# Kernel optimization log

Measured on AMD Instinct MI355X. Metric: run time of the kernel, lower is better.

The kernel has to match this reference:

```python
import jax, jax.numpy as jnp
import numpy as np

N = 100_000      # nodes
E = 1_600_000    # edges (avg degree 16)
C_IN = 32
C_OUT = 32


def setup_inputs() -> dict:
    key = jax.random.key(0)
    ks = jax.random.split(key, 8)
    x = jax.random.normal(ks[0], (N, C_IN), jnp.float32)
    edge_index = jax.random.randint(ks[1], (2, E), 0, N)
    edge_weight = jax.random.uniform(ks[2], (E,), jnp.float32)
    h = jax.random.normal(ks[3], (N, C_OUT), jnp.float32)
    s_in = 1.0 / np.sqrt(C_IN)
    s_out = 1.0 / np.sqrt(C_OUT)
    # 6 ChebConvs (gates z, r, h-tilde; each has an x-conv and an h-conv), K=2
    Wx = jax.random.normal(ks[4], (3, 2, C_IN, C_OUT), jnp.float32) * s_in
    bx = jnp.zeros((3, C_OUT), jnp.float32)
    Wh = jax.random.normal(ks[5], (3, 2, C_OUT, C_OUT), jnp.float32) * s_out
    bh = jnp.zeros((3, C_OUT), jnp.float32)
    Wl = jax.random.normal(ks[6], (C_OUT, 1), jnp.float32) * s_out
    bl = jnp.zeros((1,), jnp.float32)
    return dict(x=x, edge_index=edge_index, edge_weight=edge_weight, h=h,
                Wx=Wx, bx=bx, Wh=Wh, bh=bh, Wl=Wl, bl=bl)


def _cheb(v, W, b, coef, src, dst, n):
    # ChebConv, K=2, sym norm, lambda_max=2:
    #   T0 = v ; T1 = Lhat @ v, Lhat = -D^{-1/2} A D^{-1/2} (zero diagonal)
    t1 = jax.ops.segment_sum(coef[:, None] * v[src], dst, num_segments=n)
    return v @ W[0] + t1 @ W[1] + b


def reference(x, edge_index, edge_weight, h, Wx, bx, Wh, bh, Wl, bl):
    n = x.shape[0]
    src, dst = edge_index[0], edge_index[1]
    deg = jax.ops.segment_sum(edge_weight, src, num_segments=n)
    safe = jnp.where(deg > 0, deg, 1.0)
    dis = jnp.where(deg > 0, jax.lax.rsqrt(safe), 0.0)
    coef = -(dis[src] * edge_weight * dis[dst])  # scaled-Laplacian edge coeffs

    def gate(g, v_x, v_h):
        return (_cheb(v_x, Wx[g], bx[g], coef, src, dst, n)
                + _cheb(v_h, Wh[g], bh[g], coef, src, dst, n))

    z = jax.nn.sigmoid(gate(0, x, h))          # update gate
    r = jax.nn.sigmoid(gate(1, x, h))          # reset gate
    h_tilde = jnp.tanh(gate(2, x, h * r))      # candidate state
    h_new = z * h + (1.0 - z) * h_tilde
    out = jax.nn.softplus(jax.nn.relu(h_new) @ Wl + bl)  # [N, 1]
    return (out, h_new)
```

## Files before the change

kernel.cpp:

```cpp
#include <hip/hip_runtime.h>
#include <math.h>

#define NN 100000
#define NE 1600000
#define C  32
#define CAP 48

#define BSH    8
#define BNODES 256
#define NB     392
#define BCAP   4608
#define EPB    4096

#define WQ_SCALE 32767.0f
#define INV_WQ   (1.0f/32767.0f)
#define DEG_FIX  4194304.0f
#define INV_DEG_FIX (1.0f/4194304.0f)

typedef __attribute__((ext_vector_type(8))) short short8;
typedef __attribute__((ext_vector_type(4))) float floatx4;

__device__ __forceinline__ unsigned rn_bf16(float f) {
    unsigned b = __float_as_uint(f);
    return (b + 0x7fffu + ((b >> 16) & 1u)) >> 16;
}

__device__ __forceinline__ float sigm(float a) { return 1.f / (1.f + expf(-a)); }

__device__ __forceinline__ unsigned enc_edge(int s, float w) {
    int wq = (int)(w * WQ_SCALE + 0.5f);
    wq = wq > 32767 ? 32767 : wq;
    return ((unsigned)s << 15) | (unsigned)wq;
}

__device__ __forceinline__ short8 pack_hi8(uint4 a, uint4 b) {
    short8 v;
    v[0] = (short)(a.x >> 16); v[1] = (short)(a.y >> 16);
    v[2] = (short)(a.z >> 16); v[3] = (short)(a.w >> 16);
    v[4] = (short)(b.x >> 16); v[5] = (short)(b.y >> 16);
    v[6] = (short)(b.z >> 16); v[7] = (short)(b.w >> 16);
    return v;
}
__device__ __forceinline__ short8 pack_lo8(uint4 a, uint4 b) {
    short8 v;
    v[0] = (short)(a.x & 0xffffu); v[1] = (short)(a.y & 0xffffu);
    v[2] = (short)(a.z & 0xffffu); v[3] = (short)(a.w & 0xffffu);
    v[4] = (short)(b.x & 0xffffu); v[5] = (short)(b.y & 0xffffu);
    v[6] = (short)(b.z & 0xffffu); v[7] = (short)(b.w & 0xffffu);
    return v;
}

__global__ __launch_bounds__(256) void bin_pass(const int* __restrict__ ei,
                                                const float* __restrict__ w,
                                                int* __restrict__ gbin_d,
                                                int* __restrict__ gbin_s,
                                                uint2* __restrict__ drec,
                                                unsigned* __restrict__ srec) {
    __shared__ int hd[NB], hs[NB];
    __shared__ int sd[NB], ss[NB];
    __shared__ int bd[NB], bs[NB];
    __shared__ int cd[NB], cs[NB];
    __shared__ __align__(16) uint2 ld[EPB];
    __shared__ unsigned lsr[EPB];
    int tid = threadIdx.x;
    for (int i = tid; i < NB; i += 256) { hd[i] = 0; hs[i] = 0; }
    __syncthreads();
    int e0 = blockIdx.x * EPB;
    int m = min(EPB, NE - e0);
    for (int i = tid; i < m; i += 256) {
        atomicAdd(&hs[ei[e0 + i] >> BSH], 1);
        atomicAdd(&hd[ei[NE + e0 + i] >> BSH], 1);
    }
    __syncthreads();
    for (int i = tid; i < NB; i += 256) {
        bd[i] = hd[i] ? atomicAdd(&gbin_d[i], hd[i]) : 0;
        bs[i] = hs[i] ? atomicAdd(&gbin_s[i], hs[i]) : 0;
    }
    if (tid < 128) {
        const int* hh = (tid < 64) ? hd : hs;
        int* so = (tid < 64) ? sd : ss;
        int lane = tid & 63;
        int c0 = lane * 7;
        int vals[7]; int sum = 0;
#pragma unroll
        for (int q = 0; q < 7; ++q) {
            int idx = c0 + q;
            int v = (idx < NB) ? hh[idx] : 0;
            vals[q] = sum; sum += v;
        }
        int incl = sum;
#pragma unroll
        for (int off = 1; off < 64; off <<= 1) {
            int t = __shfl_up(incl, off, 64);
            if (lane >= off) incl += t;
        }
        int base = incl - sum;
#pragma unroll
        for (int q = 0; q < 7; ++q) {
            int idx = c0 + q;
            if (idx < NB) so[idx] = base + vals[q];
        }
    }
    __syncthreads();
    for (int i = tid; i < NB; i += 256) { cd[i] = sd[i]; cs[i] = ss[i]; }
    __syncthreads();
    for (int i = tid; i < m; i += 256) {
        int s = ei[e0 + i], d = ei[NE + e0 + i];
        float we = w[e0 + i];
        int p = atomicAdd(&cd[d >> BSH], 1);
        ld[p] = make_uint2(((unsigned)s << BSH) | (unsigned)(d & (BNODES - 1)),
                           __float_as_uint(we));
        int ps = atomicAdd(&cs[s >> BSH], 1);
        lsr[ps] = ((unsigned)(s & (BNODES - 1)) << 22) | (unsigned)(we * DEG_FIX);
    }
    __syncthreads();
    for (int i = tid; i < m; i += 256) {
        int lo = 0, hi = NB - 1;
        while (lo < hi) { int mid = (lo + hi + 1) >> 1; if (sd[mid] <= i) lo = mid; else hi = mid - 1; }
        int off = bd[lo] + (i - sd[lo]);
        if (off < BCAP) drec[(size_t)lo * BCAP + off] = ld[i];
        lo = 0; hi = NB - 1;
        while (lo < hi) { int mid = (lo + hi + 1) >> 1; if (ss[mid] <= i) lo = mid; else hi = mid - 1; }
        off = bs[lo] + (i - ss[lo]);
        if (off < BCAP) srec[(size_t)lo * BCAP + off] = lsr[i];
    }
}

__global__ __launch_bounds__(256) void bin_build(const uint2* __restrict__ drec,
                                                 const unsigned* __restrict__ srec,
                                                 const int* __restrict__ gbin_d,
                                                 const int* __restrict__ gbin_s,
                                                 const float* __restrict__ x,
                                                 const float* __restrict__ h,
                                                 unsigned* __restrict__ buckets,
                                                 int* __restrict__ cursor,
                                                 float* __restrict__ dis,
                                                 unsigned* __restrict__ xh2,
                                                 unsigned* __restrict__ xraw2) {
    __shared__ __align__(16) unsigned lbuck[BNODES * CAP];
    __shared__ int lcur[BNODES];
    __shared__ int ldeg[BNODES];
    __shared__ float sdis[BNODES];
    int b = blockIdx.x, tid = threadIdx.x;
    lcur[tid] = 0; ldeg[tid] = 0;
    __syncthreads();
    int cnt_d = min(gbin_d[b], BCAP);
    int cnt_s = min(gbin_s[b], BCAP);
    for (int i = tid; i < cnt_d; i += 256) {
        uint2 r = drec[(size_t)b * BCAP + i];
        int d8 = r.x & (BNODES - 1);
        int s  = (int)(r.x >> BSH);
        int pos = atomicAdd(&lcur[d8], 1);
        if (pos < CAP) lbuck[d8 * CAP + pos] = enc_edge(s, __uint_as_float(r.y));
    }
    for (int i = tid; i < cnt_s; i += 256) {
        unsigned r = srec[(size_t)b * BCAP + i];
        atomicAdd(&ldeg[r >> 22], (int)(r & 0x3FFFFFu));
    }
    __syncthreads();
    uint4* gb = (uint4*)(buckets + (size_t)b * BNODES * CAP);
    const uint4* lb = (const uint4*)lbuck;
    for (int i = tid; i < BNODES * CAP / 4; i += 256) gb[i] = lb[i];
    int n = b * BNODES + tid;
    float dv = 0.f;
    if (n < NN) {
        cursor[n] = lcur[tid];
        int di = ldeg[tid];
        dv = di > 0 ? rsqrtf((float)di * INV_DEG_FIX) : 0.f;
        dis[n] = dv;
    }
    sdis[tid] = dv;
    __syncthreads();
    size_t base = (size_t)b * BNODES * C;
    for (int i = tid; i < BNODES * C; i += 256) {
        size_t t = base + i;
        if (t < (size_t)NN * C) {
            float d = sdis[i >> 5];
            float xv = x[t], hv = h[t];
            xh2[t]   = (rn_bf16(xv * d) << 16) | rn_bf16(hv * d);
            xraw2[t] = (rn_bf16(xv) << 16) | rn_bf16(hv);
        }
    }
}

__global__ __launch_bounds__(256) void agg_xh(const unsigned* __restrict__ buckets,
                                              const int* __restrict__ cursor,
                                              const float* __restrict__ dis,
                                              const unsigned* __restrict__ xh2,
                                              unsigned* __restrict__ agg2) {
    int tid = threadIdx.x;
    int nl = tid >> 5, j = tid & 31;
    int n = blockIdx.x * 8 + nl;
    if (n >= NN) return;
    int cnt = min(cursor[n], CAP);
    float ax0 = 0.f, ax1 = 0.f, ax2 = 0.f, ax3 = 0.f;
    float ah0 = 0.f, ah1 = 0.f, ah2 = 0.f, ah3 = 0.f;
    for (int base = 0; base < cnt; base += 32) {
        int idx = base + j;
        int sv = 0; float cv = 0.f;
        if (idx < cnt) {
            unsigned u = buckets[(size_t)n * CAP + idx];
            sv = (int)(u >> 15);
            cv = (float)(u & 32767u) * INV_WQ;
        }
        int mm = min(32, cnt - base);
        int i2 = 0;
        for (; i2 + 8 <= mm; i2 += 8) {
            float vx[8], vh[8], cc[8];
#pragma unroll
            for (int q = 0; q < 8; ++q) {
                int s = __shfl(sv, i2 + q, 32);
                cc[q] = __shfl(cv, i2 + q, 32);
                unsigned u = xh2[(size_t)s * C + j];
                vx[q] = __uint_as_float(u & 0xffff0000u);
                vh[q] = __uint_as_float(u << 16);
            }
            ax0 = fmaf(cc[0], vx[0], ax0); ah0 = fmaf(cc[0], vh[0], ah0);
            ax1 = fmaf(cc[1], vx[1], ax1); ah1 = fmaf(cc[1], vh[1], ah1);
            ax2 = fmaf(cc[2], vx[2], ax2); ah2 = fmaf(cc[2], vh[2], ah2);
            ax3 = fmaf(cc[3], vx[3], ax3); ah3 = fmaf(cc[3], vh[3], ah3);
            ax0 = fmaf(cc[4], vx[4], ax0); ah0 = fmaf(cc[4], vh[4], ah0);
            ax1 = fmaf(cc[5], vx[5], ax1); ah1 = fmaf(cc[5], vh[5], ah1);
            ax2 = fmaf(cc[6], vx[6], ax2); ah2 = fmaf(cc[6], vh[6], ah2);
            ax3 = fmaf(cc[7], vx[7], ax3); ah3 = fmaf(cc[7], vh[7], ah3);
        }
        for (; i2 < mm; ++i2) {
            int s = __shfl(sv, i2, 32); float cf = __shfl(cv, i2, 32);
            unsigned u = xh2[(size_t)s * C + j];
            ax0 = fmaf(cf, __uint_as_float(u & 0xffff0000u), ax0);
            ah0 = fmaf(cf, __uint_as_float(u << 16), ah0);
        }
    }
    float disn = -dis[n];
    float ax = disn * ((ax0 + ax1) + (ax2 + ax3));
    float ah = disn * ((ah0 + ah1) + (ah2 + ah3));
    agg2[(size_t)n * C + j] = (rn_bf16(ax) << 16) | rn_bf16(ah);
}

__global__ __launch_bounds__(256) void gate_mfma(const unsigned* __restrict__ xraw2,
                                                 const unsigned* __restrict__ agg2,
                                                 const float* __restrict__ dis,
                                                 const float* __restrict__ Wx,
                                                 const float* __restrict__ Wh,
                                                 const float* __restrict__ bx,
                                                 const float* __restrict__ bh,
                                                 unsigned* __restrict__ hrz2,
                                                 unsigned short* __restrict__ hr16,
                                                 float* __restrict__ pout) {
    __shared__ __align__(16) unsigned short Bl[20][64][8];
    int tid = threadIdx.x;
    for (int i = tid; i < 20 * 64; i += 256) {
        int f = i >> 6, l = i & 63;
        int t, c;
        if (f < 16) { t = f >> 2; c = f & 3; }
        else        { t = 4 + ((f - 16) >> 1); c = (f - 16) & 1; }
        int g = t >> 1;
        int j = ((t & 1) << 4) + (l & 15);
        int kb = (l >> 4) << 3;
        const float* srcp = (c < 2 ? Wx : Wh) + g * 2048 + (c & 1) * 1024 + j;
        unsigned pk[4];
#pragma unroll
        for (int q = 0; q < 4; ++q) {
            unsigned lo = rn_bf16(srcp[(kb + 2 * q) * 32]);
            unsigned hi = rn_bf16(srcp[(kb + 2 * q + 1) * 32]);
            pk[q] = (hi << 16) | lo;
        }
        *(uint4*)(&Bl[f][l][0]) = make_uint4(pk[0], pk[1], pk[2], pk[3]);
    }

    int lane = tid & 63, wave = tid >> 6;
    int j0 = lane & 15, quad = lane >> 4;
    int tbase = blockIdx.x * 64 + wave * 16;
    int na = tbase + j0;
    short8 A0 = {0,0,0,0,0,0,0,0}, A1 = A0, A2 = A0, A3 = A0;
    if (na < NN) {
        const uint4* px = (const uint4*)(xraw2 + (size_t)na * C + quad * 8);
        uint4 xa = px[0], xb = px[1];
        A0 = pack_hi8(xa, xb);
        A2 = pack_lo8(xa, xb);
        const uint4* pg = (const uint4*)(agg2 + (size_t)na * C + quad * 8);
        uint4 ga = pg[0], gb = pg[1];
        A1 = pack_hi8(ga, gb);
        A3 = pack_lo8(ga, gb);
    }
    __syncthreads();

#define B8(f) (*(const short8*)(&Bl[f][lane][0]))
    floatx4 az0 = {0.f,0.f,0.f,0.f}, az1 = az0, ar0 = az0, ar1 = az0, ap0 = az0, ap1 = az0;
    az0 = __builtin_amdgcn_mfma_f32_16x16x32_bf16(A0, B8(0),  az0, 0, 0, 0);
    az0 = __builtin_amdgcn_mfma_f32_16x16x32_bf16(A1, B8(1),  az0, 0, 0, 0);
    az0 = __builtin_amdgcn_mfma_f32_16x16x32_bf16(A2, B8(2),  az0, 0, 0, 0);
    az0 = __builtin_amdgcn_mfma_f32_16x16x32_bf16(A3, B8(3),  az0, 0, 0, 0);
    az1 = __builtin_amdgcn_mfma_f32_16x16x32_bf16(A0, B8(4),  az1, 0, 0, 0);
    az1 = __builtin_amdgcn_mfma_f32_16x16x32_bf16(A1, B8(5),  az1, 0, 0, 0);
    az1 = __builtin_amdgcn_mfma_f32_16x16x32_bf16(A2, B8(6),  az1, 0, 0, 0);
    az1 = __builtin_amdgcn_mfma_f32_16x16x32_bf16(A3, B8(7),  az1, 0, 0, 0);
    ar0 = __builtin_amdgcn_mfma_f32_16x16x32_bf16(A0, B8(8),  ar0, 0, 0, 0);
    ar0 = __builtin_amdgcn_mfma_f32_16x16x32_bf16(A1, B8(9),  ar0, 0, 0, 0);
    ar0 = __builtin_amdgcn_mfma_f32_16x16x32_bf16(A2, B8(10), ar0, 0, 0, 0);
    ar0 = __builtin_amdgcn_mfma_f32_16x16x32_bf16(A3, B8(11), ar0, 0, 0, 0);
    ar1 = __builtin_amdgcn_mfma_f32_16x16x32_bf16(A0, B8(12), ar1, 0, 0, 0);
    ar1 = __builtin_amdgcn_mfma_f32_16x16x32_bf16(A1, B8(13), ar1, 0, 0, 0);
    ar1 = __builtin_amdgcn_mfma_f32_16x16x32_bf16(A2, B8(14), ar1, 0, 0, 0);
    ar1 = __builtin_amdgcn_mfma_f32_16x16x32_bf16(A3, B8(15), ar1, 0, 0, 0);
    ap0 = __builtin_amdgcn_mfma_f32_16x16x32_bf16(A0, B8(16), ap0, 0, 0, 0);
    ap0 = __builtin_amdgcn_mfma_f32_16x16x32_bf16(A1, B8(17), ap0, 0, 0, 0);
    ap1 = __builtin_amdgcn_mfma_f32_16x16x32_bf16(A0, B8(18), ap1, 0, 0, 0);
    ap1 = __builtin_amdgcn_mfma_f32_16x16x32_bf16(A1, B8(19), ap1, 0, 0, 0);
#undef B8

    float bza = bx[j0]      + bh[j0];
    float bzb = bx[j0 + 16] + bh[j0 + 16];
    float bra = bx[32 + j0] + bh[32 + j0];
    float brb = bx[48 + j0] + bh[48 + j0];
    float bpa = bx[64 + j0] + bh[64 + j0];
    float bpb = bx[80 + j0] + bh[80 + j0];
#pragma unroll
    for (int p = 0; p < 4; ++p) {
        int nr = tbase + quad * 4 + p;
        if (nr >= NN) continue;
        float dn = dis[nr];
        size_t ra = (size_t)nr * C + j0;
        size_t rb = ra + 16;
        float ha = __uint_as_float(xraw2[ra] << 16);
        float hb = __uint_as_float(xraw2[rb] << 16);
        float za  = sigm(az0[p] + bza);
        float zb  = sigm(az1[p] + bzb);
        float rav = sigm(ar0[p] + bra);
        float rbv = sigm(ar1[p] + brb);
        float hra = ha * rav, hrb = hb * rbv;
        hrz2[ra] = (rn_bf16(hra) << 16) | rn_bf16(za);
        hrz2[rb] = (rn_bf16(hrb) << 16) | rn_bf16(zb);
        hr16[ra] = (unsigned short)rn_bf16(dn * hra);
        hr16[rb] = (unsigned short)rn_bf16(dn * hrb);
        pout[ra] = ap0[p] + bpa;
        pout[rb] = ap1[p] + bpb;
    }
}

__global__ __launch_bounds__(256) void final_kernel(const float* __restrict__ h,
                                                    const unsigned* __restrict__ hrz2,
                                                    const float* __restrict__ ph,
                                                    const unsigned* __restrict__ buckets,
                                                    const int* __restrict__ cursor,
                                                    const float* __restrict__ dis,
                                                    const unsigned short* __restrict__ hr16,
                                                    const float* __restrict__ Wh,
                                                    const float* __restrict__ Wl,
                                                    const float* __restrict__ bl,
                                                    float* __restrict__ out,
                                                    float* __restrict__ hnew) {
    __shared__ float sW[2 * 1024];
    __shared__ float sIn[2][8][C];
    int tid = threadIdx.x;
    for (int i = tid; i < 2 * 1024; i += 256) sW[i] = Wh[4096 + i];
    int nl = tid >> 5, j = tid & 31;
    int n = blockIdx.x * 8 + nl;
    if (n >= NN) return;

    int cnt = min(cursor[n], CAP);
    float a0 = 0.f, a1 = 0.f, a2 = 0.f, a3 = 0.f;
    for (int base = 0; base < cnt; base += 32) {
        int idx = base + j;
        int sv = 0; float cv = 0.f;
        if (idx < cnt) {
            unsigned u = buckets[(size_t)n * CAP + idx];
            sv = (int)(u >> 15);
            cv = (float)(u & 32767u) * INV_WQ;
        }
        int mm = min(32, cnt - base);
        int i2 = 0;
        for (; i2 + 8 <= mm; i2 += 8) {
            float vv[8], cc[8];
#pragma unroll
            for (int q = 0; q < 8; ++q) {
                int s = __shfl(sv, i2 + q, 32);
                cc[q] = __shfl(cv, i2 + q, 32);
                vv[q] = __uint_as_float(((unsigned)hr16[(size_t)s * C + j]) << 16);
            }
            a0 = fmaf(cc[0], vv[0], a0);
            a1 = fmaf(cc[1], vv[1], a1);
            a2 = fmaf(cc[2], vv[2], a2);
            a3 = fmaf(cc[3], vv[3], a3);
            a0 = fmaf(cc[4], vv[4], a0);
            a1 = fmaf(cc[5], vv[5], a1);
            a2 = fmaf(cc[6], vv[6], a2);
            a3 = fmaf(cc[7], vv[7], a3);
        }
        for (; i2 < mm; ++i2) {
            int s = __shfl(sv, i2, 32); float cf = __shfl(cv, i2, 32);
            a0 = fmaf(cf, __uint_as_float(((unsigned)hr16[(size_t)s * C + j]) << 16), a0);
        }
    }
    float ag = -dis[n] * ((a0 + a1) + (a2 + a3));
    unsigned uz = hrz2[(size_t)n * C + j];
    float hrv = __uint_as_float(uz & 0xffff0000u);
    float zv  = __uint_as_float(uz << 16);
    sIn[0][nl][j] = hrv;
    sIn[1][nl][j] = ag;
    __syncthreads();

    float acc = ph[(size_t)n * C + j];
#pragma unroll
    for (int k = 0; k < C; ++k) {
        int o = k * 32 + j;
        acc = fmaf(sIn[0][nl][k], sW[o], acc);
        acc = fmaf(sIn[1][nl][k], sW[1024 + o], acc);
    }
    float ht = tanhf(acc);
    float hv = h[(size_t)n * C + j];
    float hn = fmaf(zv, hv - ht, ht);
    hnew[(size_t)n * C + j] = hn;
    float p = fmaxf(hn, 0.f) * Wl[j];
#pragma unroll
    for (int off = 16; off; off >>= 1) p += __shfl_down(p, off, 32);
    if (j == 0) {
        float v = p + bl[0];
        out[n] = fmaxf(v, 0.f) + log1pf(expf(-fabsf(v)));
    }
}

extern "C" void kernel_launch(void* const* d_in, const int* in_sizes, int n_in,
                              void* d_out, int out_size, void* d_ws, size_t ws_size,
                              hipStream_t stream) {
    const float* x  = (const float*)d_in[0];
    const int*   ei = (const int*)d_in[1];
    const float* ew = (const float*)d_in[2];
    const float* h  = (const float*)d_in[3];
    const float* Wx = (const float*)d_in[4];
    const float* bx = (const float*)d_in[5];
    const float* Wh = (const float*)d_in[6];
    const float* bh = (const float*)d_in[7];
    const float* Wl = (const float*)d_in[8];
    const float* bl = (const float*)d_in[9];

    float* out  = (float*)d_out;
    float* hnew = out + NN;

    char* ws = (char*)d_ws;
    int*            gbin_d = (int*)ws;
    int*            gbin_s = gbin_d + NB;
    uint2*          drec   = (uint2*)(ws + 4096);
    unsigned*       srec   = (unsigned*)(drec + (size_t)NB * BCAP);
    unsigned*       buckets= srec + (size_t)NB * BCAP;
    int*            cursor = (int*)(buckets + (size_t)NB * BNODES * CAP);
    float*          dis    = (float*)(cursor + NN);
    unsigned*       xh2    = (unsigned*)(dis + NN);
    unsigned*       xraw2  = xh2 + (size_t)NN * C;
    unsigned*       agg2   = xraw2 + (size_t)NN * C;
    float*          pbuf   = (float*)(agg2 + (size_t)NN * C);
    unsigned short* hr16   = (unsigned short*)srec;
    unsigned*       hrz2   = xh2;

    hipMemsetAsync(d_ws, 0, 4096, stream);

    bin_pass    <<<(NE + EPB - 1) / EPB, 256, 0, stream>>>(ei, ew, gbin_d, gbin_s,
                                                           drec, srec);
    bin_build   <<<NB, 256, 0, stream>>>(drec, srec, gbin_d, gbin_s, x, h,
                                         buckets, cursor, dis, xh2, xraw2);
    agg_xh      <<<(NN + 7) / 8, 256, 0, stream>>>(buckets, cursor, dis, xh2, agg2);
    gate_mfma   <<<(NN + 63) / 64, 256, 0, stream>>>(xraw2, agg2, dis, Wx, Wh,
                                                     bx, bh, hrz2, hr16, pbuf);
    final_kernel<<<(NN + 7) / 8, 256, 0, stream>>>(h, hrz2, pbuf,
                                                   buckets, cursor, dis, hr16,
                                                   Wh, Wl, bl, out, hnew);
}
```

Measured before the change: 302.7 us.

## Split hr gather into two 16-channel planes and move x/h packing to own kernel

The hr*r feature is now stored as two separate 16-channel bf16 planes and gathered in two passes, each half-warp handling a different edge, so each gather pass touches a smaller 3.2 MB working set that is more likely to stay cache-resident. The x/h bf16 packing moves out of bin_build into a separate elementwise kernel, which shrinks bin_build and lets the packing run at full-grid parallelism. The cost is two extra kernel launches, a second pass over the edge buckets, and a float intermediate buffer for the first half. Grids now use NN/8 with no bounds check, which is safe only because NN is divisible by 8.

```diff
diff --git a/kernel.cpp b/kernel.cpp
--- a/kernel.cpp
+++ b/kernel.cpp
@@ -130,17 +130,12 @@
                                                  const unsigned* __restrict__ srec,
                                                  const int* __restrict__ gbin_d,
                                                  const int* __restrict__ gbin_s,
-                                                 const float* __restrict__ x,
-                                                 const float* __restrict__ h,
                                                  unsigned* __restrict__ buckets,
                                                  int* __restrict__ cursor,
-                                                 float* __restrict__ dis,
-                                                 unsigned* __restrict__ xh2,
-                                                 unsigned* __restrict__ xraw2) {
+                                                 float* __restrict__ dis) {
     __shared__ __align__(16) unsigned lbuck[BNODES * CAP];
     __shared__ int lcur[BNODES];
     __shared__ int ldeg[BNODES];
-    __shared__ float sdis[BNODES];
     int b = blockIdx.x, tid = threadIdx.x;
     lcur[tid] = 0; ldeg[tid] = 0;
     __syncthreads();
@@ -162,25 +157,24 @@
     const uint4* lb = (const uint4*)lbuck;
     for (int i = tid; i < BNODES * CAP / 4; i += 256) gb[i] = lb[i];
     int n = b * BNODES + tid;
-    float dv = 0.f;
     if (n < NN) {
         cursor[n] = lcur[tid];
         int di = ldeg[tid];
-        dv = di > 0 ? rsqrtf((float)di * INV_DEG_FIX) : 0.f;
-        dis[n] = dv;
-    }
-    sdis[tid] = dv;
-    __syncthreads();
-    size_t base = (size_t)b * BNODES * C;
-    for (int i = tid; i < BNODES * C; i += 256) {
-        size_t t = base + i;
-        if (t < (size_t)NN * C) {
-            float d = sdis[i >> 5];
-            float xv = x[t], hv = h[t];
-            xh2[t]   = (rn_bf16(xv * d) << 16) | rn_bf16(hv * d);
-            xraw2[t] = (rn_bf16(xv) << 16) | rn_bf16(hv);
-        }
-    }
+        dis[n] = di > 0 ? rsqrtf((float)di * INV_DEG_FIX) : 0.f;
+    }
+}
+
+__global__ __launch_bounds__(256) void build_xh(const float* __restrict__ x,
+                                                const float* __restrict__ h,
+                                                const float* __restrict__ dis,
+                                                unsigned* __restrict__ xh2,
+                                                unsigned* __restrict__ xraw2) {
+    int t = blockIdx.x * 256 + threadIdx.x;
+    if (t >= NN * C) return;
+    float d = dis[t >> 5];
+    float xv = x[t], hv = h[t];
+    xh2[t]   = (rn_bf16(xv * d) << 16) | rn_bf16(hv * d);
+    xraw2[t] = (rn_bf16(xv) << 16) | rn_bf16(hv);
 }
 
 __global__ __launch_bounds__(256) void agg_xh(const unsigned* __restrict__ buckets,
@@ -245,7 +239,7 @@
                                                  const float* __restrict__ bx,
                                                  const float* __restrict__ bh,
                                                  unsigned* __restrict__ hrz2,
-                                                 unsigned short* __restrict__ hr16,
+                                                 unsigned short* __restrict__ hrpl,
                                                  float* __restrict__ pout) {
     __shared__ __align__(16) unsigned short Bl[20][64][8];
     int tid = threadIdx.x;
@@ -331,33 +325,22 @@
         float hra = ha * rav, hrb = hb * rbv;
         hrz2[ra] = (rn_bf16(hra) << 16) | rn_bf16(za);
         hrz2[rb] = (rn_bf16(hrb) << 16) | rn_bf16(zb);
-        hr16[ra] = (unsigned short)rn_bf16(dn * hra);
-        hr16[rb] = (unsigned short)rn_bf16(dn * hrb);
+        hrpl[(size_t)nr * 16 + j0]            = (unsigned short)rn_bf16(dn * hra);
+        hrpl[(size_t)NN * 16 + nr * 16 + j0]  = (unsigned short)rn_bf16(dn * hrb);
         pout[ra] = ap0[p] + bpa;
         pout[rb] = ap1[p] + bpb;
     }
 }
 
-__global__ __launch_bounds__(256) void final_kernel(const float* __restrict__ h,
-                                                    const unsigned* __restrict__ hrz2,
-                                                    const float* __restrict__ ph,
-                                                    const unsigned* __restrict__ buckets,
-                                                    const int* __restrict__ cursor,
-                                                    const float* __restrict__ dis,
-                                                    const unsigned short* __restrict__ hr16,
-                                                    const float* __restrict__ Wh,
-                                                    const float* __restrict__ Wl,
-                                                    const float* __restrict__ bl,
-                                                    float* __restrict__ out,
-                                                    float* __restrict__ hnew) {
-    __shared__ float sW[2 * 1024];
-    __shared__ float sIn[2][8][C];
+__global__ __launch_bounds__(256) void hr_gather(const unsigned* __restrict__ buckets,
+                                                 const int* __restrict__ cursor,
+                                                 const float* __restrict__ dis,
+                                                 const unsigned short* __restrict__ hrP,
+                                                 float* __restrict__ aggP) {
     int tid = threadIdx.x;
-    for (int i = tid; i < 2 * 1024; i += 256) sW[i] = Wh[4096 + i];
     int nl = tid >> 5, j = tid & 31;
     int n = blockIdx.x * 8 + nl;
-    if (n >= NN) return;
-
+    int sub = j >> 4, c = j & 15;
     int cnt = min(cursor[n], CAP);
     float a0 = 0.f, a1 = 0.f, a2 = 0.f, a3 = 0.f;
     for (int base = 0; base < cnt; base += 32) {
@@ -369,35 +352,98 @@
             cv = (float)(u & 32767u) * INV_WQ;
         }
         int mm = min(32, cnt - base);
-        int i2 = 0;
-        for (; i2 + 8 <= mm; i2 += 8) {
-            float vv[8], cc[8];
-#pragma unroll
-            for (int q = 0; q < 8; ++q) {
-                int s = __shfl(sv, i2 + q, 32);
-                cc[q] = __shfl(cv, i2 + q, 32);
-                vv[q] = __uint_as_float(((unsigned)hr16[(size_t)s * C + j]) << 16);
+        int steps = (mm + 1) >> 1;
+        int t = 0;
+        for (; t + 4 <= steps; t += 4) {
+            float vv[4], cc[4];
+#pragma unroll
+            for (int q = 0; q < 4; ++q) {
+                int el = 2 * (t + q) + sub;
+                int s = __shfl(sv, el, 32);
+                cc[q] = __shfl(cv, el, 32);
+                vv[q] = __uint_as_float(((unsigned)hrP[(size_t)s * 16 + c]) << 16);
             }
             a0 = fmaf(cc[0], vv[0], a0);
             a1 = fmaf(cc[1], vv[1], a1);
             a2 = fmaf(cc[2], vv[2], a2);
             a3 = fmaf(cc[3], vv[3], a3);
-            a0 = fmaf(cc[4], vv[4], a0);
-            a1 = fmaf(cc[5], vv[5], a1);
-            a2 = fmaf(cc[6], vv[6], a2);
-            a3 = fmaf(cc[7], vv[7], a3);
-        }
-        for (; i2 < mm; ++i2) {
-            int s = __shfl(sv, i2, 32); float cf = __shfl(cv, i2, 32);
-            a0 = fmaf(cf, __uint_as_float(((unsigned)hr16[(size_t)s * C + j]) << 16), a0);
-        }
-    }
-    float ag = -dis[n] * ((a0 + a1) + (a2 + a3));
+        }
+        for (; t < steps; ++t) {
+            int el = 2 * t + sub;
+            int s = __shfl(sv, el, 32);
+            float cf = __shfl(cv, el, 32);
+            a0 = fmaf(cf, __uint_as_float(((unsigned)hrP[(size_t)s * 16 + c]) << 16), a0);
+        }
+    }
+    float tot = (a0 + a1) + (a2 + a3);
+    tot += __shfl_down(tot, 16, 32);
+    if (sub == 0) aggP[(size_t)n * 16 + c] = -dis[n] * tot;
+}
+
+__global__ __launch_bounds__(256) void hr_gatherB_finish(const float* __restrict__ h,
+                                                         const unsigned* __restrict__ hrz2,
+                                                         const float* __restrict__ ph,
+                                                         const unsigned* __restrict__ buckets,
+                                                         const int* __restrict__ cursor,
+                                                         const float* __restrict__ dis,
+                                                         const unsigned short* __restrict__ hrB,
+                                                         const float* __restrict__ aggA,
+                                                         const float* __restrict__ Wh,
+                                                         const float* __restrict__ Wl,
+                                                         const float* __restrict__ bl,
+                                                         float* __restrict__ out,
+                                                         float* __restrict__ hnew) {
+    __shared__ float sW[2 * 1024];
+    __shared__ float sIn[2][8][C];
+    int tid = threadIdx.x;
+    for (int i = tid; i < 2 * 1024; i += 256) sW[i] = Wh[4096 + i];
+    int nl = tid >> 5, j = tid & 31;
+    int n = blockIdx.x * 8 + nl;
+    int sub = j >> 4, c = j & 15;
+
+    int cnt = min(cursor[n], CAP);
+    float a0 = 0.f, a1 = 0.f, a2 = 0.f, a3 = 0.f;
+    for (int base = 0; base < cnt; base += 32) {
+        int idx = base + j;
+        int sv = 0; float cv = 0.f;
+        if (idx < cnt) {
+            unsigned u = buckets[(size_t)n * CAP + idx];
+            sv = (int)(u >> 15);
+            cv = (float)(u & 32767u) * INV_WQ;
+        }
+        int mm = min(32, cnt - base);
+        int steps = (mm + 1) >> 1;
+        int t = 0;
+        for (; t + 4 <= steps; t += 4) {
+            float vv[4], cc[4];
+#pragma unroll
+            for (int q = 0; q < 4; ++q) {
+                int el = 2 * (t + q) + sub;
+                int s = __shfl(sv, el, 32);
+                cc[q] = __shfl(cv, el, 32);
+                vv[q] = __uint_as_float(((unsigned)hrB[(size_t)s * 16 + c]) << 16);
+            }
+            a0 = fmaf(cc[0], vv[0], a0);
+            a1 = fmaf(cc[1], vv[1], a1);
+            a2 = fmaf(cc[2], vv[2], a2);
+            a3 = fmaf(cc[3], vv[3], a3);
+        }
+        for (; t < steps; ++t) {
+            int el = 2 * t + sub;
+            int s = __shfl(sv, el, 32);
+            float cf = __shfl(cv, el, 32);
+            a0 = fmaf(cf, __uint_as_float(((unsigned)hrB[(size_t)s * 16 + c]) << 16), a0);
+        }
+    }
+    float tot = (a0 + a1) + (a2 + a3);
+    tot += __shfl_down(tot, 16, 32);
+
     unsigned uz = hrz2[(size_t)n * C + j];
     float hrv = __uint_as_float(uz & 0xffff0000u);
     float zv  = __uint_as_float(uz << 16);
     sIn[0][nl][j] = hrv;
-    sIn[1][nl][j] = ag;
+    if (sub == 0) sIn[1][nl][16 + c] = -dis[n] * tot;
+    else          sIn[1][nl][c]      = aggA[(size_t)n * 16 + c];
     __syncthreads();
 
     float acc = ph[(size_t)n * C + j];
@@ -449,19 +495,22 @@
     unsigned*       xraw2  = xh2 + (size_t)NN * C;
     unsigned*       agg2   = xraw2 + (size_t)NN * C;
     float*          pbuf   = (float*)(agg2 + (size_t)NN * C);
-    unsigned short* hr16   = (unsigned short*)srec;
+    unsigned short* hrpl   = (unsigned short*)srec;
+    float*          aggA   = (float*)drec;
     unsigned*       hrz2   = xh2;
 
     hipMemsetAsync(d_ws, 0, 4096, stream);
 
-    bin_pass    <<<(NE + EPB - 1) / EPB, 256, 0, stream>>>(ei, ew, gbin_d, gbin_s,
-                                                           drec, srec);
-    bin_build   <<<NB, 256, 0, stream>>>(drec, srec, gbin_d, gbin_s, x, h,
-                                         buckets, cursor, dis, xh2, xraw2);
-    agg_xh      <<<(NN + 7) / 8, 256, 0, stream>>>(buckets, cursor, dis, xh2, agg2);
-    gate_mfma   <<<(NN + 63) / 64, 256, 0, stream>>>(xraw2, agg2, dis, Wx, Wh,
-                                                     bx, bh, hrz2, hr16, pbuf);
-    final_kernel<<<(NN + 7) / 8, 256, 0, stream>>>(h, hrz2, pbuf,
-                                                   buckets, cursor, dis, hr16,
-                                                   Wh, Wl, bl, out, hnew);
-}
+    bin_pass        <<<(NE + EPB - 1) / EPB, 256, 0, stream>>>(ei, ew, gbin_d, gbin_s,
+                                                               drec, srec);
+    bin_build       <<<NB, 256, 0, stream>>>(drec, srec, gbin_d, gbin_s,
+                                             buckets, cursor, dis);
+    build_xh        <<<(NN * C + 255) / 256, 256, 0, stream>>>(x, h, dis, xh2, xraw2);
+    agg_xh          <<<(NN + 7) / 8, 256, 0, stream>>>(buckets, cursor, dis, xh2, agg2);
+    gate_mfma       <<<(NN + 63) / 64, 256, 0, stream>>>(xraw2, agg2, dis, Wx, Wh,
+                                                         bx, bh, hrz2, hrpl, pbuf);
+    hr_gather       <<<NN / 8, 256, 0, stream>>>(buckets, cursor, dis, hrpl, aggA);
+    hr_gatherB_finish<<<NN / 8, 256, 0, stream>>>(h, hrz2, pbuf, buckets, cursor, dis,
+                                                  hrpl + (size_t)NN * 16, aggA,
+                                                  Wh, Wl, bl, out, hnew);
+}
```

New measurement: 300.6 us. No clear change (-0.7%).

## Compact per-node edge buckets into CSR layout with global bin offsets

Applied to the files above, without the earlier changes.

Replaces the fixed-capacity padded per-node buckets (CAP slots per node) with a compacted CSR-style array. A new single-wave scan kernel computes per-bin offsets, and bin_build does an in-block prefix sum to place each node's edges contiguously. This cuts the bucket write traffic from NN*CAP words to about NE words and tightens the reads in the two aggregation kernels. The x/h bf16 packing moves into a separate elementwise kernel, EPB is halved to launch more binning blocks, and the change adds two extra launches plus a binary search per edge during compaction.

```diff
diff --git a/kernel.cpp b/kernel.cpp
--- a/kernel.cpp
+++ b/kernel.cpp
@@ -10,7 +10,7 @@
 #define BNODES 256
 #define NB     392
 #define BCAP   4608
-#define EPB    4096
+#define EPB    2048
 
 #define WQ_SCALE 32767.0f
 #define INV_WQ   (1.0f/32767.0f)
@@ -126,21 +126,45 @@
     }
 }
 
+__global__ __launch_bounds__(64) void scan_bins(const int* __restrict__ gbin_d,
+                                                int* __restrict__ binoff) {
+    int lane = threadIdx.x;
+    int c0 = lane * 7;
+    int vals[7]; int sum = 0;
+#pragma unroll
+    for (int q = 0; q < 7; ++q) {
+        int idx = c0 + q;
+        int v = (idx < NB) ? min(gbin_d[idx], BCAP) : 0;
+        vals[q] = sum; sum += v;
+    }
+    int incl = sum;
+#pragma unroll
+    for (int off = 1; off < 64; off <<= 1) {
+        int t = __shfl_up(incl, off, 64);
+        if (lane >= off) incl += t;
+    }
+    int base = incl - sum;
+#pragma unroll
+    for (int q = 0; q < 7; ++q) {
+        int idx = c0 + q;
+        if (idx < NB) binoff[idx] = base + vals[q];
+    }
+}
+
 __global__ __launch_bounds__(256) void bin_build(const uint2* __restrict__ drec,
                                                  const unsigned* __restrict__ srec,
                                                  const int* __restrict__ gbin_d,
                                                  const int* __restrict__ gbin_s,
-                                                 const float* __restrict__ x,
-                                                 const float* __restrict__ h,
+                                                 const int* __restrict__ binoff,
                                                  unsigned* __restrict__ buckets,
-                                                 int* __restrict__ cursor,
-                                                 float* __restrict__ dis,
-                                                 unsigned* __restrict__ xh2,
-                                                 unsigned* __restrict__ xraw2) {
+                                                 int* __restrict__ starts,
+                                                 int* __restrict__ cnts,
+                                                 float* __restrict__ dis) {
     __shared__ __align__(16) unsigned lbuck[BNODES * CAP];
     __shared__ int lcur[BNODES];
     __shared__ int ldeg[BNODES];
-    __shared__ float sdis[BNODES];
+    __shared__ int nodeoff[BNODES];
+    __shared__ int wsum[4];
     int b = blockIdx.x, tid = threadIdx.x;
     lcur[tid] = 0; ldeg[tid] = 0;
     __syncthreads();
@@ -158,33 +182,52 @@
         atomicAdd(&ldeg[r >> 22], (int)(r & 0x3FFFFFu));
     }
     __syncthreads();
-    uint4* gb = (uint4*)(buckets + (size_t)b * BNODES * CAP);
-    const uint4* lb = (const uint4*)lbuck;
-    for (int i = tid; i < BNODES * CAP / 4; i += 256) gb[i] = lb[i];
+    int myc = min(lcur[tid], CAP);
+    int lane = tid & 63, wv = tid >> 6;
+    int inc = myc;
+#pragma unroll
+    for (int off = 1; off < 64; off <<= 1) {
+        int t = __shfl_up(inc, off, 64);
+        if (lane >= off) inc += t;
+    }
+    if (lane == 63) wsum[wv] = inc;
+    __syncthreads();
+    if (tid == 0) { int a = 0; for (int q = 0; q < 4; ++q) { int v = wsum[q]; wsum[q] = a; a += v; } }
+    __syncthreads();
+    nodeoff[tid] = wsum[wv] + inc - myc;
+    __syncthreads();
+    int gbase = binoff[b];
+    int total = nodeoff[BNODES - 1] + min(lcur[BNODES - 1], CAP);
+    for (int i = tid; i < total; i += 256) {
+        int lo = 0, hi = BNODES - 1;
+        while (lo < hi) { int mid = (lo + hi + 1) >> 1; if (nodeoff[mid] <= i) lo = mid; else hi = mid - 1; }
+        buckets[(size_t)gbase + i] = lbuck[lo * CAP + (i - nodeoff[lo])];
+    }
     int n = b * BNODES + tid;
-    float dv = 0.f;
     if (n < NN) {
-        cursor[n] = lcur[tid];
+        starts[n] = gbase + nodeoff[tid];
+        cnts[n] = myc;
         int di = ldeg[tid];
-        dv = di > 0 ? rsqrtf((float)di * INV_DEG_FIX) : 0.f;
-        dis[n] = dv;
-    }
-    sdis[tid] = dv;
-    __syncthreads();
-    size_t base = (size_t)b * BNODES * C;
-    for (int i = tid; i < BNODES * C; i += 256) {
-        size_t t = base + i;
-        if (t < (size_t)NN * C) {
-            float d = sdis[i >> 5];
-            float xv = x[t], hv = h[t];
-            xh2[t]   = (rn_bf16(xv * d) << 16) | rn_bf16(hv * d);
-            xraw2[t] = (rn_bf16(xv) << 16) | rn_bf16(hv);
-        }
-    }
+        dis[n] = di > 0 ? rsqrtf((float)di * INV_DEG_FIX) : 0.f;
+    }
+}
+
+__global__ __launch_bounds__(256) void build_xh(const float* __restrict__ x,
+                                                const float* __restrict__ h,
+                                                const float* __restrict__ dis,
+                                                unsigned* __restrict__ xh2,
+                                                unsigned* __restrict__ xraw2) {
+    int t = blockIdx.x * 256 + threadIdx.x;
+    if (t >= NN * C) return;
+    float d = dis[t >> 5];
+    float xv = x[t], hv = h[t];
+    xh2[t]   = (rn_bf16(xv * d) << 16) | rn_bf16(hv * d);
+    xraw2[t] = (rn_bf16(xv) << 16) | rn_bf16(hv);
 }
 
 __global__ __launch_bounds__(256) void agg_xh(const unsigned* __restrict__ buckets,
-                                              const int* __restrict__ cursor,
+                                              const int* __restrict__ starts,
+                                              const int* __restrict__ cnts,
                                               const float* __restrict__ dis,
                                               const unsigned* __restrict__ xh2,
                                               unsigned* __restrict__ agg2) {
@@ -192,14 +235,15 @@
     int nl = tid >> 5, j = tid & 31;
     int n = blockIdx.x * 8 + nl;
     if (n >= NN) return;
-    int cnt = min(cursor[n], CAP);
+    int s0 = starts[n];
+    int cnt = cnts[n];
     float ax0 = 0.f, ax1 = 0.f, ax2 = 0.f, ax3 = 0.f;
     float ah0 = 0.f, ah1 = 0.f, ah2 = 0.f, ah3 = 0.f;
     for (int base = 0; base < cnt; base += 32) {
         int idx = base + j;
         int sv = 0; float cv = 0.f;
         if (idx < cnt) {
-            unsigned u = buckets[(size_t)n * CAP + idx];
+            unsigned u = buckets[(size_t)s0 + idx];
             sv = (int)(u >> 15);
             cv = (float)(u & 32767u) * INV_WQ;
         }
@@ -342,7 +386,8 @@
                                                     const unsigned* __restrict__ hrz2,
                                                     const float* __restrict__ ph,
                                                     const unsigned* __restrict__ buckets,
-                                                    const int* __restrict__ cursor,
+                                                    const int* __restrict__ starts,
+                                                    const int* __restrict__ cnts,
                                                     const float* __restrict__ dis,
                                                     const unsigned short* __restrict__ hr16,
                                                     const float* __restrict__ Wh,
@@ -358,13 +403,14 @@
     int n = blockIdx.x * 8 + nl;
     if (n >= NN) return;
 
-    int cnt = min(cursor[n], CAP);
+    int s0v = starts[n];
+    int cnt = cnts[n];
     float a0 = 0.f, a1 = 0.f, a2 = 0.f, a3 = 0.f;
     for (int base = 0; base < cnt; base += 32) {
         int idx = base + j;
         int sv = 0; float cv = 0.f;
         if (idx < cnt) {
-            unsigned u = buckets[(size_t)n * CAP + idx];
+            unsigned u = buckets[(size_t)s0v + idx];
             sv = (int)(u >> 15);
             cv = (float)(u & 32767u) * INV_WQ;
         }
@@ -440,11 +486,13 @@
     char* ws = (char*)d_ws;
     int*            gbin_d = (int*)ws;
     int*            gbin_s = gbin_d + NB;
-    uint2*          drec   = (uint2*)(ws + 4096);
+    int*            binoff = gbin_s + NB;
+    uint2*          drec   = (uint2*)(ws + 8192);
     unsigned*       srec   = (unsigned*)(drec + (size_t)NB * BCAP);
     unsigned*       buckets= srec + (size_t)NB * BCAP;
-    int*            cursor = (int*)(buckets + (size_t)NB * BNODES * CAP);
-    float*          dis    = (float*)(cursor + NN);
+    int*            starts = (int*)(buckets + NE);
+    int*            cnts   = starts + NN;
+    float*          dis    = (float*)(cnts + NN);
     unsigned*       xh2    = (unsigned*)(dis + NN);
     unsigned*       xraw2  = xh2 + (size_t)NN * C;
     unsigned*       agg2   = xraw2 + (size_t)NN * C;
@@ -456,12 +504,15 @@
 
     bin_pass    <<<(NE + EPB - 1) / EPB, 256, 0, stream>>>(ei, ew, gbin_d, gbin_s,
                                                            drec, srec);
-    bin_build   <<<NB, 256, 0, stream>>>(drec, srec, gbin_d, gbin_s, x, h,
-                                         buckets, cursor, dis, xh2, xraw2);
-    agg_xh      <<<(NN + 7) / 8, 256, 0, stream>>>(buckets, cursor, dis, xh2, agg2);
+    scan_bins   <<<1, 64, 0, stream>>>(gbin_d, binoff);
+    bin_build   <<<NB, 256, 0, stream>>>(drec, srec, gbin_d, gbin_s, binoff,
+                                         buckets, starts, cnts, dis);
+    build_xh    <<<(NN * C + 255) / 256, 256, 0, stream>>>(x, h, dis, xh2, xraw2);
+    agg_xh      <<<(NN + 7) / 8, 256, 0, stream>>>(buckets, starts, cnts, dis,
+                                                   xh2, agg2);
     gate_mfma   <<<(NN + 63) / 64, 256, 0, stream>>>(xraw2, agg2, dis, Wx, Wh,
                                                      bx, bh, hrz2, hr16, pbuf);
-    final_kernel<<<(NN + 7) / 8, 256, 0, stream>>>(h, hrz2, pbuf,
-                                                   buckets, cursor, dis, hr16,
+    final_kernel<<<(NN + 7) / 8, 256, 0, stream>>>(h, hrz2, pbuf, buckets, starts,
+                                                   cnts, dis, hr16,
                                                    Wh, Wl, bl, out, hnew);
 }
```

Result: no change. 300.2 us (-0.8%).
